# Kernel tuning notes

Measured on AMD Instinct MI355X. Metric: run time of the kernel, lower is better.

Reference implementation:

```python
import jax, jax.numpy as jnp
import numpy as np

N_NODES = 20000
N_EDGES = 320000
F_IN = 256      # num_features_mol
HIDDEN = 512    # hidden_size


def _glorot(key, shape):
    fan_in, fan_out = shape
    lim = jnp.sqrt(6.0 / (fan_in + fan_out)).astype(jnp.float32)
    return jax.random.uniform(key, shape, jnp.float32, -lim, lim)


def setup_inputs() -> dict:
    key = jax.random.key(0)
    ks = jax.random.split(key, 12)
    x = jax.random.normal(ks[0], (N_NODES, F_IN), jnp.float32)
    edge_index = jax.random.randint(ks[1], (2, N_EDGES), 0, N_NODES, dtype=jnp.int64)
    d1, d2, d3 = F_IN * 2, F_IN * 2, F_IN * 4  # 512, 512, 1024
    return {
        "x": x,
        "edge_index": edge_index,
        # SAGEConv layer i: lin_l (neighbor, with bias), lin_r (root, no bias)
        "Wl1": _glorot(ks[2], (F_IN, d1)), "bl1": jnp.zeros((d1,), jnp.float32),
        "Wr1": _glorot(ks[3], (F_IN, d1)),
        "Wl2": _glorot(ks[4], (d1, d2)), "bl2": jnp.zeros((d2,), jnp.float32),
        "Wr2": _glorot(ks[5], (d1, d2)),
        "Wl3": _glorot(ks[6], (d2, d3)), "bl3": jnp.zeros((d3,), jnp.float32),
        "Wr3": _glorot(ks[7], (d2, d3)),
        # mol_fc_g1: Linear(4*F -> hidden)
        "Wfc": _glorot(ks[8], (d3, HIDDEN)), "bfc": jnp.zeros((HIDDEN,), jnp.float32),
    }


def _sage_mean(x, src, dst, Wl, bl, Wr):
    # mean-aggregate neighbor features: messages flow src -> dst
    msg = x[src]                                               # [E, d]
    agg = jax.ops.segment_sum(msg, dst, num_segments=N_NODES)  # [N, d]
    cnt = jax.ops.segment_sum(jnp.ones((src.shape[0],), x.dtype), dst,
                              num_segments=N_NODES)            # [N]
    mean = agg / jnp.maximum(cnt, 1.0)[:, None]                # zero-deg -> 0
    return mean @ Wl + bl + x @ Wr


def reference(x, edge_index, Wl1, bl1, Wr1, Wl2, bl2, Wr2, Wl3, bl3, Wr3, Wfc, bfc):
    src, dst = edge_index[0], edge_index[1]
    h = jax.nn.relu(_sage_mean(x, src, dst, Wl1, bl1, Wr1))
    h = jax.nn.relu(_sage_mean(h, src, dst, Wl2, bl2, Wr2))
    h = jax.nn.relu(_sage_mean(h, src, dst, Wl3, bl3, Wr3))
    return h @ Wfc + bfc                                       # [N, HIDDEN]
```

## Files before the change

kernel.cpp:

```cpp
#include <hip/hip_runtime.h>
#include <hip/hip_bf16.h>


typedef __bf16 bf16x8 __attribute__((ext_vector_type(8)));
typedef float  f32x4  __attribute__((ext_vector_type(4)));

#define N_NODES 20000
#define N_EDGES 320000
#define MPAD 20096

__device__ __forceinline__ int clampi(int v, int lo, int hi) {
    return v < lo ? lo : (v > hi ? hi : v);
}

__device__ __forceinline__ void load16_lds(const void* g, void* l) {
    __builtin_amdgcn_global_load_lds(
        (const __attribute__((address_space(1))) void*)g,
        (__attribute__((address_space(3))) void*)l, 16, 0, 0);
}


struct TDesc { const float* W; __bf16* Wt; int K, N, KT, koff, tile0; };
struct TDescs { TDesc d[7]; };

__global__ void k_prep(TDescs ds, const float* __restrict__ x,
                       __bf16* __restrict__ xrm, __bf16* __restrict__ acat,
                       const int* __restrict__ ei, int* __restrict__ cnt) {
    __shared__ float tile[32][33];
    int b = blockIdx.x;
    int tid = threadIdx.y * 32 + threadIdx.x;

    if (b < 2304) {
        int di = 0;
#pragma unroll
        for (int i = 1; i < 7; ++i)
            if (b >= ds.d[i].tile0) di = i;
        const float* W = ds.d[di].W;
        __bf16* Wt = ds.d[di].Wt;
        int N = ds.d[di].N, KT = ds.d[di].KT, koff = ds.d[di].koff;
        int t = b - ds.d[di].tile0;
        int ntn = N >> 5;
        int nb = (t % ntn) * 32, kb = (t / ntn) * 32;
        for (int i = 0; i < 32; i += 8) {
            int k = kb + threadIdx.y + i, n = nb + threadIdx.x;
            tile[threadIdx.y + i][threadIdx.x] = W[(size_t)k * N + n];
        }
        __syncthreads();
        for (int i = 0; i < 32; i += 8) {
            int n = nb + threadIdx.y + i, k = koff + kb + threadIdx.x;
            size_t o = (size_t)(n >> 7) * ((size_t)KT * 128) + (size_t)(k >> 3) * 1024 +
                       (size_t)((n & 127) * 8) + (k & 7);
            Wt[o] = (__bf16)tile[threadIdx.x][threadIdx.y + i];
        }
    } else if (b < 4804) {
        int node = (b - 2304) * 8 + (tid >> 5);
        int f0 = (tid & 31) * 8;
        float4 u = *(const float4*)(x + (size_t)node * 256 + f0);
        float4 w = *(const float4*)(x + (size_t)node * 256 + f0 + 4);
        alignas(16) __bf16 tmp[8] = {(__bf16)u.x, (__bf16)u.y, (__bf16)u.z, (__bf16)u.w,
                                     (__bf16)w.x, (__bf16)w.y, (__bf16)w.z, (__bf16)w.w};
        *(uint4*)(xrm + (size_t)node * 256 + f0) = *(const uint4*)tmp;
        *(uint4*)(acat + (size_t)(node >> 7) * (512 * 128) +
                  (size_t)(32 + (f0 >> 3)) * 1024 + (size_t)((node & 127) * 8)) =
            *(const uint4*)tmp;
    } else {
        int e = (b - 4804) * 256 + tid;
        atomicAdd(&cnt[clampi(ei[N_EDGES + e], 0, N_NODES - 1)], 1);
    }
}


__global__ __launch_bounds__(1024) void k_scan_block(const int* __restrict__ cnt,
                                                     int* __restrict__ off,
                                                     int* __restrict__ bsum, int n) {
    __shared__ int sm[1024];
    int b = blockIdx.x, tid = threadIdx.x;
    int i = b * 1024 + tid;
    int v = (i < n) ? cnt[i] : 0;
    sm[tid] = v;
    __syncthreads();
    for (int s = 1; s < 1024; s <<= 1) {
        int t = (tid >= s) ? sm[tid - s] : 0;
        __syncthreads();
        sm[tid] += t;
        __syncthreads();
    }
    if (i < n) off[i] = sm[tid] - v;
    if (tid == 1023) bsum[b] = sm[1023];
}

__global__ __launch_bounds__(1024) void k_scan_add(int* __restrict__ off,
                                                   int* __restrict__ cur,
                                                   const int* __restrict__ bsum, int n) {
    int b = blockIdx.x;
    int carry = 0;
    for (int j = 0; j < b; ++j) carry += bsum[j];
    int i = b * 1024 + threadIdx.x;
    if (i < n) {
        int v = off[i] + carry;
        off[i] = v;
        cur[i] = v;
    }
    if (b == 0 && threadIdx.x == 0) off[n] = N_EDGES;
}

__global__ void k_fill(const int* __restrict__ ei, int E,
                       int* __restrict__ cur, int* __restrict__ csr) {
    int e = blockIdx.x * blockDim.x + threadIdx.x;
    if (e < E) {
        int dst = clampi(ei[E + e], 0, N_NODES - 1);
        int src = clampi(ei[e], 0, N_NODES - 1);
        int pos = atomicAdd(&cur[dst], 1);
        if (pos >= 0 && pos < E) csr[pos] = src;
    }
}


template <int D, int KC>
__global__ __launch_bounds__(256) void k_agg(const __hip_bfloat16* __restrict__ hrm,
                                             const int* __restrict__ off,
                                             const int* __restrict__ csr,
                                             __bf16* __restrict__ acat) {
    constexpr int FPL = D / 64;
    int wave = threadIdx.x >> 6, lane = threadIdx.x & 63;
    int node = blockIdx.x * 4 + wave;
    int c0 = lane * FPL;
    int beg = off[node], end = off[node + 1];
    float a[FPL] = {};

    if constexpr (FPL == 8) {
        auto ldrow = [&](int s) { return *(const uint4*)(hrm + (size_t)s * D + c0); };
        auto addv = [&](uint4 v) {
            const __hip_bfloat16* hb = (const __hip_bfloat16*)&v;
#pragma unroll
            for (int j = 0; j < 8; ++j) a[j] += __bfloat162float(hb[j]);
        };
        int e = beg;
        for (; e + 3 < end; e += 4) {
            int s0 = csr[e], s1 = csr[e + 1], s2 = csr[e + 2], s3 = csr[e + 3];
            uint4 v0 = ldrow(s0), v1 = ldrow(s1), v2 = ldrow(s2), v3 = ldrow(s3);
            addv(v0); addv(v1); addv(v2); addv(v3);
        }
        for (; e < end; ++e) addv(ldrow(csr[e]));
    } else {
        auto ldrow = [&](int s) { return *(const uint2*)(hrm + (size_t)s * D + c0); };
        auto addv = [&](uint2 v) {
            const __hip_bfloat16* hb = (const __hip_bfloat16*)&v;
#pragma unroll
            for (int j = 0; j < 4; ++j) a[j] += __bfloat162float(hb[j]);
        };
        int e = beg;
        for (; e + 3 < end; e += 4) {
            int s0 = csr[e], s1 = csr[e + 1], s2 = csr[e + 2], s3 = csr[e + 3];
            uint2 v0 = ldrow(s0), v1 = ldrow(s1), v2 = ldrow(s2), v3 = ldrow(s3);
            addv(v0); addv(v1); addv(v2); addv(v3);
        }
        for (; e < end; ++e) addv(ldrow(csr[e]));
    }

    float inv = 1.f / fmaxf((float)(end - beg), 1.f);
    alignas(16) __bf16 tmp[FPL];
#pragma unroll
    for (int j = 0; j < FPL; ++j) tmp[j] = (__bf16)(a[j] * inv);

    __bf16* base = acat + (size_t)(node >> 7) * ((size_t)KC * 128) +
                   (size_t)((node & 127) * 8);
    if constexpr (FPL == 8) {
        *(uint4*)(base + (size_t)lane * 1024) = *(const uint4*)tmp;
    } else {
        *(uint2*)(base + (size_t)(lane >> 1) * 1024 + (size_t)((lane & 1) * 4)) =
            *(const uint2*)tmp;
    }
}


template <bool RELU, int OUTMODE, int MT>
__global__ __launch_bounds__(256) void k_gemm(const __bf16* __restrict__ A, int K, int M,
                                              const __bf16* __restrict__ B,
                                              const float* __restrict__ bias,
                                              __bf16* __restrict__ osw, int Kc, int coff,
                                              __bf16* __restrict__ orm, int ldrm,
                                              float* __restrict__ of32, int ldf,
                                              int rtiles, int ctlog2) {
    constexpr int MREP = MT / 32;
    constexpr int STAGE = MT * 128 + 16384;
    __shared__ char smem[2 * STAGE];

    int bid = blockIdx.x;
    int xcd = bid & 7, local = bid >> 3;
    int cmask = (1 << ctlog2) - 1;
    int colTile = local & cmask;
    int rowTile = (local >> ctlog2) * 8 + xcd;
    if (rowTile >= rtiles) return;

    int panel = (MT == 128) ? rowTile : (rowTile >> 1);
    int half  = (MT == 128) ? 0 : (rowTile & 1);

    const __bf16* Abase = A + (size_t)panel * ((size_t)K * 128) + half * 512;
    const __bf16* Btile = B + (size_t)colTile * ((size_t)K * 128);

    int tid = threadIdx.x;
    int wave = tid >> 6, lane = tid & 63;
    int wr = wave >> 1, wc = wave & 1;
    int quad = lane >> 4, l16 = lane & 15;

    f32x4 acc[MREP][4] = {};
    const int nt = K >> 6;

    auto stage = [&](int buf, int t) {
        __bf16* Al = (__bf16*)(smem + buf * STAGE);
        __bf16* Bl = (__bf16*)(smem + buf * STAGE + MT * 128);
#pragma unroll
        for (int j = 0; j < MT / 32; ++j) {
            int s = j * 256 + tid;
            int c = s / MT, w = s % MT;
            load16_lds(Abase + (size_t)(t * 8 + c) * 1024 + w * 8, Al + s * 8);
        }
        const __bf16* gB = Btile + (size_t)t * 64 * 128;
#pragma unroll
        for (int j = 0; j < 4; ++j) {
            int slot = (j * 256 + tid) * 8;
            load16_lds(gB + slot, Bl + slot);
        }
    };

    stage(0, 0);
    __syncthreads();
    int cur = 0;
    for (int t = 0; t < nt; ++t) {
        if (t + 1 < nt) stage(cur ^ 1, t + 1);
        const __bf16* Al = (const __bf16*)(smem + cur * STAGE);
        const __bf16* Bl = (const __bf16*)(smem + cur * STAGE + MT * 128);
#pragma unroll
        for (int sp = 0; sp < 2; ++sp) {
            bf16x8 af[MREP], bf[4];
#pragma unroll
            for (int mi = 0; mi < MREP; ++mi)
                af[mi] = *(const bf16x8*)(Al + (sp * 4 + quad) * (MT * 8) +
                                          (wr * (MT / 2) + mi * 16 + l16) * 8);
#pragma unroll
            for (int ni = 0; ni < 4; ++ni)
                bf[ni] = *(const bf16x8*)(Bl + sp * 4096 + quad * 1024 +
                                          (wc * 64 + ni * 16 + l16) * 8);
#pragma unroll
            for (int mi = 0; mi < MREP; ++mi)
#pragma unroll
                for (int ni = 0; ni < 4; ++ni)
                    acc[mi][ni] = __builtin_amdgcn_mfma_f32_16x16x32_bf16(
                        af[mi], bf[ni], acc[mi][ni], 0, 0, 0);
        }
        __syncthreads();
        cur ^= 1;
    }

    int col0 = colTile * 128;
    int row0 = rowTile * MT;

    if (OUTMODE != 2) {
        __bf16* cb = (__bf16*)smem;
#pragma unroll
        for (int ni = 0; ni < 4; ++ni) {
            int ct = wc * 64 + ni * 16 + l16;
            float bv = bias[col0 + ct];
#pragma unroll
            for (int mi = 0; mi < MREP; ++mi) {
                int rb = wr * (MT / 2) + mi * 16 + quad * 4;
#pragma unroll
                for (int r = 0; r < 4; ++r) {
                    float v = acc[mi][ni][r] + bv;
                    if (RELU) v = fmaxf(v, 0.f);
                    cb[(ct >> 3) * (MT * 8) + (rb + r) * 8 + (ct & 7)] = (__bf16)v;
                }
            }
        }
        __syncthreads();
        __bf16* dst = osw + (size_t)panel * ((size_t)Kc * 128) +
                      (size_t)((coff + col0) >> 3) * 1024 + half * 512;
#pragma unroll
        for (int p2 = 0; p2 < MT / 16; ++p2) {
            int s = p2 * 256 + tid;
            int cc = s / MT, w = s % MT;
            *(uint4*)(dst + (size_t)cc * 1024 + w * 8) = *(const uint4*)(cb + s * 8);
        }
        if (OUTMODE == 1) {
#pragma unroll
            for (int p2 = 0; p2 < MT / 16; ++p2) {
                int rr = p2 * 16 + (tid >> 4);
                int cc = tid & 15;
                *(uint4*)(orm + (size_t)(row0 + rr) * ldrm + col0 + cc * 8) =
                    *(const uint4*)(cb + cc * (MT * 8) + rr * 8);
            }
        }
    } else {
        float* cf = (float*)smem;
#pragma unroll
        for (int h = 0; h < 2; ++h) {
            if (wc == h) {
#pragma unroll
                for (int ni = 0; ni < 4; ++ni) {
                    int ctl = ni * 16 + l16;
                    float bv = bias[col0 + h * 64 + ctl];
#pragma unroll
                    for (int mi = 0; mi < MREP; ++mi) {
                        int rb = wr * (MT / 2) + mi * 16 + quad * 4;
#pragma unroll
                        for (int r = 0; r < 4; ++r) {
                            float v = acc[mi][ni][r] + bv;
                            if (RELU) v = fmaxf(v, 0.f);
                            cf[(rb + r) * 68 + ctl] = v;
                        }
                    }
                }
            }
            __syncthreads();
            int chunk = tid & 15, rl = tid >> 4;
#pragma unroll
            for (int p2 = 0; p2 < MT / 16; ++p2) {
                int rt = p2 * 16 + rl;
                int row = row0 + rt;
                if (row < M) {
                    float4 v = *(const float4*)(cf + rt * 68 + chunk * 4);
                    *(float4*)(of32 + (size_t)row * ldf + col0 + h * 64 + chunk * 4) = v;
                }
            }
            __syncthreads();
        }
    }
}


extern "C" void kernel_launch(void* const* d_in, const int* in_sizes, int n_in,
                              void* d_out, int out_size, void* d_ws, size_t ws_size,
                              hipStream_t stream) {
    const float* x   = (const float*)d_in[0];
    const int*   ei  = (const int*)d_in[1];
    const float* Wl1 = (const float*)d_in[2];
    const float* bl1 = (const float*)d_in[3];
    const float* Wr1 = (const float*)d_in[4];
    const float* Wl2 = (const float*)d_in[5];
    const float* bl2 = (const float*)d_in[6];
    const float* Wr2 = (const float*)d_in[7];
    const float* Wl3 = (const float*)d_in[8];
    const float* bl3 = (const float*)d_in[9];
    const float* Wr3 = (const float*)d_in[10];
    const float* Wfc = (const float*)d_in[11];
    const float* bfc = (const float*)d_in[12];
    float* out = (float*)d_out;

    const int NN = N_NODES, E = N_EDGES;
    const int NB = (NN + 1023) / 1024;

    char* p = (char*)d_ws;
    auto alloc = [&](size_t bytes) {
        char* r = p;
        p += (bytes + 511) & ~(size_t)511;
        return r;
    };
    int* cnt   = (int*)alloc((size_t)NN * 4);
    int* off   = (int*)alloc((size_t)(NN + 1) * 4);
    int* cur   = (int*)alloc((size_t)NN * 4);
    int* csr   = (int*)alloc((size_t)E * 4);
    int* bsum  = (int*)alloc((size_t)NB * 4);
    __bf16* Acat1 = (__bf16*)alloc((size_t)MPAD * 512 * 2);
    __bf16* Acat2 = (__bf16*)alloc((size_t)MPAD * 1024 * 2);
    __bf16* Acat3 = (__bf16*)alloc((size_t)MPAD * 1024 * 2);
    __bf16* Hrm   = (__bf16*)alloc((size_t)MPAD * 512 * 2);
    __bf16* Xrm   = (__bf16*)alloc((size_t)MPAD * 256 * 2);
    __bf16* Wt1 = (__bf16*)alloc((size_t)512 * 512 * 2);
    __bf16* Wt2 = (__bf16*)alloc((size_t)512 * 1024 * 2);
    __bf16* Wt3 = (__bf16*)alloc((size_t)1024 * 1024 * 2);
    __bf16* Wt4 = (__bf16*)alloc((size_t)512 * 1024 * 2);
    __bf16* H3 = Acat2;

    hipMemsetAsync(cnt, 0, (size_t)NN * 4, stream);
    TDescs td;
    td.d[0] = {Wl1, Wt1, 256, 512, 512, 0, 0};
    td.d[1] = {Wr1, Wt1, 256, 512, 512, 256, 128};
    td.d[2] = {Wl2, Wt2, 512, 512, 1024, 0, 256};
    td.d[3] = {Wr2, Wt2, 512, 512, 1024, 512, 512};
    td.d[4] = {Wl3, Wt3, 512, 1024, 1024, 0, 768};
    td.d[5] = {Wr3, Wt3, 512, 1024, 1024, 512, 1280};
    td.d[6] = {Wfc, Wt4, 1024, 512, 1024, 0, 1792};
    k_prep<<<6054, dim3(32, 8), 0, stream>>>(td, x, Xrm, Acat1, ei, cnt);

    k_scan_block<<<NB, 1024, 0, stream>>>(cnt, off, bsum, NN);
    k_scan_add<<<NB, 1024, 0, stream>>>(off, cur, bsum, NN);
    k_fill<<<(E + 255) / 256, 256, 0, stream>>>(ei, E, cur, csr);

    int rt128 = (NN + 127) / 128;
    int rg128 = ((rt128 + 7) / 8) * 8;
    int rt64  = MPAD / 64;
    int rg64  = ((rt64 + 7) / 8) * 8;

    k_agg<256, 512><<<NN / 4, 256, 0, stream>>>(
        (const __hip_bfloat16*)Xrm, off, csr, Acat1);
    k_gemm<true, 1, 64><<<rg64 * 4, 256, 0, stream>>>(
        Acat1, 512, NN, Wt1, bl1, Acat2, 1024, 512, Hrm, 512, nullptr, 0, rt64, 2);

    k_agg<512, 1024><<<NN / 4, 256, 0, stream>>>(
        (const __hip_bfloat16*)Hrm, off, csr, Acat2);
    k_gemm<true, 1, 64><<<rg64 * 4, 256, 0, stream>>>(
        Acat2, 1024, NN, Wt2, bl2, Acat3, 1024, 512, Hrm, 512, nullptr, 0, rt64, 2);

    k_agg<512, 1024><<<NN / 4, 256, 0, stream>>>(
        (const __hip_bfloat16*)Hrm, off, csr, Acat3);
    k_gemm<true, 0, 128><<<rg128 * 8, 256, 0, stream>>>(
        Acat3, 1024, NN, Wt3, bl3, H3, 1024, 0, nullptr, 0, nullptr, 0, rt128, 3);

    k_gemm<false, 2, 64><<<rg64 * 4, 256, 0, stream>>>(
        H3, 1024, NN, Wt4, bfc, nullptr, 0, 0, nullptr, 0, out, 512, rt64, 2);
}
```

Before: 394.5 us.

## Split aggregation by column groups per XCD with edge-parallel lanes and shuffle reduction

Rewrites the mean-aggregation kernel so each block handles one eighth of the feature columns for 16 nodes, with the column group chosen by blockIdx&7. Each wave's lanes are split across edges as well as columns, so neighbor rows load in parallel, and partial sums are combined with xor shuffles. The aim is to keep each column slice of the feature matrix resident in one XCD's L2 and to raise memory-level parallelism on the gathers. The cost is extra shuffle work, more csr index reads (each column group rereads them), and lanes left idle on low-degree nodes.

```diff
diff --git a/kernel.cpp b/kernel.cpp
--- a/kernel.cpp
+++ b/kernel.cpp
@@ -117,59 +117,45 @@
 
 
 template <int D, int KC>
-__global__ __launch_bounds__(256) void k_agg(const __hip_bfloat16* __restrict__ hrm,
-                                             const int* __restrict__ off,
-                                             const int* __restrict__ csr,
-                                             __bf16* __restrict__ acat) {
-    constexpr int FPL = D / 64;
+__global__ __launch_bounds__(256) void k_agg_x(const __hip_bfloat16* __restrict__ hrm,
+                                               const int* __restrict__ off,
+                                               const int* __restrict__ csr,
+                                               __bf16* __restrict__ acat) {
+    constexpr int CG = D / 8;
+    constexpr int L  = CG / 8;
+    constexpr int R  = 64 / L;
+    int g = blockIdx.x & 7;
+    int nb = blockIdx.x >> 3;
     int wave = threadIdx.x >> 6, lane = threadIdx.x & 63;
-    int node = blockIdx.x * 4 + wave;
-    int c0 = lane * FPL;
-    int beg = off[node], end = off[node + 1];
-    float a[FPL] = {};
-
-    if constexpr (FPL == 8) {
-        auto ldrow = [&](int s) { return *(const uint4*)(hrm + (size_t)s * D + c0); };
-        auto addv = [&](uint4 v) {
+    int r = lane / L, c = lane % L;
+    int col0 = g * CG + c * 8;
+
+#pragma unroll
+    for (int i = 0; i < 4; ++i) {
+        int node = nb * 16 + wave * 4 + i;
+        int beg = off[node], end = off[node + 1];
+        float a[8] = {};
+        for (int e = beg + r; e < end; e += R) {
+            int s = csr[e];
+            uint4 v = *(const uint4*)(hrm + (size_t)s * D + col0);
             const __hip_bfloat16* hb = (const __hip_bfloat16*)&v;
 #pragma unroll
             for (int j = 0; j < 8; ++j) a[j] += __bfloat162float(hb[j]);
-        };
-        int e = beg;
-        for (; e + 3 < end; e += 4) {
-            int s0 = csr[e], s1 = csr[e + 1], s2 = csr[e + 2], s3 = csr[e + 3];
-            uint4 v0 = ldrow(s0), v1 = ldrow(s1), v2 = ldrow(s2), v3 = ldrow(s3);
-            addv(v0); addv(v1); addv(v2); addv(v3);
-        }
-        for (; e < end; ++e) addv(ldrow(csr[e]));
-    } else {
-        auto ldrow = [&](int s) { return *(const uint2*)(hrm + (size_t)s * D + c0); };
-        auto addv = [&](uint2 v) {
-            const __hip_bfloat16* hb = (const __hip_bfloat16*)&v;
-#pragma unroll
-            for (int j = 0; j < 4; ++j) a[j] += __bfloat162float(hb[j]);
-        };
-        int e = beg;
-        for (; e + 3 < end; e += 4) {
-            int s0 = csr[e], s1 = csr[e + 1], s2 = csr[e + 2], s3 = csr[e + 3];
-            uint2 v0 = ldrow(s0), v1 = ldrow(s1), v2 = ldrow(s2), v3 = ldrow(s3);
-            addv(v0); addv(v1); addv(v2); addv(v3);
-        }
-        for (; e < end; ++e) addv(ldrow(csr[e]));
-    }
-
-    float inv = 1.f / fmaxf((float)(end - beg), 1.f);
-    alignas(16) __bf16 tmp[FPL];
-#pragma unroll
-    for (int j = 0; j < FPL; ++j) tmp[j] = (__bf16)(a[j] * inv);
-
-    __bf16* base = acat + (size_t)(node >> 7) * ((size_t)KC * 128) +
-                   (size_t)((node & 127) * 8);
-    if constexpr (FPL == 8) {
-        *(uint4*)(base + (size_t)lane * 1024) = *(const uint4*)tmp;
-    } else {
-        *(uint2*)(base + (size_t)(lane >> 1) * 1024 + (size_t)((lane & 1) * 4)) =
-            *(const uint2*)tmp;
+        }
+#pragma unroll
+        for (int m = L; m < 64; m <<= 1)
+#pragma unroll
+            for (int j = 0; j < 8; ++j) a[j] += __shfl_xor(a[j], m, 64);
+        if (lane < L) {
+            float inv = 1.f / fmaxf((float)(end - beg), 1.f);
+            alignas(16) __bf16 tmp[8];
+#pragma unroll
+            for (int j = 0; j < 8; ++j) tmp[j] = (__bf16)(a[j] * inv);
+            int chunk = g * L + c;
+            *(uint4*)(acat + (size_t)(node >> 7) * ((size_t)KC * 128) +
+                      (size_t)chunk * 1024 + (size_t)((node & 127) * 8)) =
+                *(const uint4*)tmp;
+        }
     }
 }
 
@@ -391,18 +377,19 @@
     int rg128 = ((rt128 + 7) / 8) * 8;
     int rt64  = MPAD / 64;
     int rg64  = ((rt64 + 7) / 8) * 8;
-
-    k_agg<256, 512><<<NN / 4, 256, 0, stream>>>(
+    const int aggGrid = (NN / 16) * 8;
+
+    k_agg_x<256, 512><<<aggGrid, 256, 0, stream>>>(
         (const __hip_bfloat16*)Xrm, off, csr, Acat1);
     k_gemm<true, 1, 64><<<rg64 * 4, 256, 0, stream>>>(
         Acat1, 512, NN, Wt1, bl1, Acat2, 1024, 512, Hrm, 512, nullptr, 0, rt64, 2);
 
-    k_agg<512, 1024><<<NN / 4, 256, 0, stream>>>(
+    k_agg_x<512, 1024><<<aggGrid, 256, 0, stream>>>(
         (const __hip_bfloat16*)Hrm, off, csr, Acat2);
     k_gemm<true, 1, 64><<<rg64 * 4, 256, 0, stream>>>(
         Acat2, 1024, NN, Wt2, bl2, Acat3, 1024, 512, Hrm, 512, nullptr, 0, rt64, 2);
 
-    k_agg<512, 1024><<<NN / 4, 256, 0, stream>>>(
+    k_agg_x<512, 1024><<<aggGrid, 256, 0, stream>>>(
         (const __hip_bfloat16*)Hrm, off, csr, Acat3);
     k_gemm<true, 0, 128><<<rg128 * 8, 256, 0, stream>>>(
         Acat3, 1024, NN, Wt3, bl3, H3, 1024, 0, nullptr, 0, nullptr, 0, rt128, 3);
```

After: 429.6 us. 8.9% more time.
